# Optimization experiments

Hardware: AMD Instinct MI355X
Metric: run time of the kernel (lower is better)

The kernel has to match this reference:

```python
import jax, jax.numpy as jnp
from jax import lax
import numpy as np
import math

B, H, W = 4, 64, 64
D_MODEL, D_STATE, D_CONV, EXPAND, K = 96, 16, 3, 2, 4
D_INNER = EXPAND * D_MODEL          # 192
DT_RANK = math.ceil(D_MODEL / 16)   # 6


def setup_inputs() -> dict:
    key = jax.random.key(0)
    ks = jax.random.split(key, 12)
    s = 0.02
    rgb = jax.random.normal(ks[0], (B, H, W, D_MODEL), jnp.float32)
    t = jax.random.normal(ks[1], (B, H, W, D_MODEL), jnp.float32)
    in_proj1_w = jax.random.normal(ks[2], (2 * D_INNER, D_MODEL), jnp.float32) * s
    in_proj2_w = jax.random.normal(ks[3], (2 * D_INNER, D_MODEL), jnp.float32) * s
    conv1_w = jax.random.normal(ks[4], (D_INNER, 1, D_CONV, D_CONV), jnp.float32) * s
    conv1_b = jnp.zeros((D_INNER,), jnp.float32)
    conv2_w = jax.random.normal(ks[5], (D_INNER, 1, D_CONV, D_CONV), jnp.float32) * s
    conv2_b = jnp.zeros((D_INNER,), jnp.float32)
    x_proj_weight = jax.random.normal(ks[6], (K, DT_RANK + 2 * D_STATE, D_INNER), jnp.float32) * s
    lim = DT_RANK ** -0.5
    dt_projs_weight = jax.random.uniform(ks[7], (K, D_INNER, DT_RANK), jnp.float32, -lim, lim)
    dt = jnp.exp(jax.random.uniform(ks[8], (K, D_INNER), jnp.float32)
                 * (math.log(0.1) - math.log(0.001)) + math.log(0.001))
    dt = jnp.clip(dt, 1e-4, None)
    dt_projs_bias = dt + jnp.log(-jnp.expm1(-dt))  # inverse softplus
    A_logs = jnp.tile(jnp.log(jnp.arange(1, D_STATE + 1, dtype=jnp.float32))[None], (K * D_INNER, 1))
    Ds = jnp.ones((K * D_INNER,), jnp.float32)
    norm1_w = jnp.ones((D_INNER,), jnp.float32); norm1_b = jnp.zeros((D_INNER,), jnp.float32)
    norm2_w = jnp.ones((D_INNER,), jnp.float32); norm2_b = jnp.zeros((D_INNER,), jnp.float32)
    out_proj1_w = jax.random.normal(ks[9], (D_MODEL, D_INNER), jnp.float32) * s
    out_proj2_w = jax.random.normal(ks[10], (D_MODEL, D_INNER), jnp.float32) * s
    return dict(rgb=rgb, t=t, in_proj1_w=in_proj1_w, in_proj2_w=in_proj2_w,
                conv1_w=conv1_w, conv1_b=conv1_b, conv2_w=conv2_w, conv2_b=conv2_b,
                x_proj_weight=x_proj_weight, dt_projs_weight=dt_projs_weight,
                dt_projs_bias=dt_projs_bias, A_logs=A_logs, Ds=Ds,
                norm1_w=norm1_w, norm1_b=norm1_b, norm2_w=norm2_w, norm2_b=norm2_b,
                out_proj1_w=out_proj1_w, out_proj2_w=out_proj2_w)


def _dwconv(x, w, b):
    # x: (B, C, H, W), depthwise 3x3, padding=1
    y = lax.conv_general_dilated(x, w, (1, 1), 'SAME',
                                 feature_group_count=x.shape[1],
                                 dimension_numbers=('NCHW', 'OIHW', 'NCHW'))
    return y + b[None, :, None, None]


def _ln(x, w, b, eps=1e-5):
    m = x.mean(-1, keepdims=True)
    v = ((x - m) ** 2).mean(-1, keepdims=True)
    return (x - m) / jnp.sqrt(v + eps) * w + b


def _cross_scan(x):
    # x: (B, C, H, W) -> (B, 4, C, L): row-major, col-major, and their reverses
    Bz, C, Hh, Ww = x.shape
    L = Hh * Ww
    xr = x.reshape(Bz, C, L)
    xt = x.transpose(0, 1, 3, 2).reshape(Bz, C, L)
    xh = jnp.stack([xr, xt], 1)                        # (B,2,C,L)
    return jnp.concatenate([xh, jnp.flip(xh, -1)], 1)  # (B,4,C,L)


def _cross_merge(y, Hh, Ww):
    # y: (B, 4, C, L) -> (B, C, L); undo scan directions then sum
    Bz, _, C, L = y.shape
    inv = jnp.flip(y[:, 2:4], -1)                      # (B,2,C,L)
    wh = y[:, 1].reshape(Bz, C, Ww, Hh).transpose(0, 1, 3, 2).reshape(Bz, C, L)
    invwh = inv[:, 1].reshape(Bz, C, Ww, Hh).transpose(0, 1, 3, 2).reshape(Bz, C, L)
    return y[:, 0] + inv[:, 0] + wh + invwh


def _selective_scan(u, delta, A, Bs, Cs, Ds, delta_bias):
    # u, delta: (B, K, C, L2); A: (K, C, N); Bs, Cs: (B, K, N, L2); Ds: (K, C)
    Bz, Kk, C, L2 = u.shape
    N = A.shape[-1]
    delta = jax.nn.softplus(delta + delta_bias[None, :, :, None])

    def step(h, inp):
        d_l, u_l, B_l, C_l = inp               # (B,K,C),(B,K,C),(B,K,N),(B,K,N)
        dA = jnp.exp(d_l[..., None] * A[None])            # (B,K,C,N)
        dBu = (d_l * u_l)[..., None] * B_l[:, :, None, :]  # (B,K,C,N)
        h = h * dA + dBu
        y = jnp.einsum('bkcn,bkn->bkc', h, C_l)
        return h, y

    h0 = jnp.zeros((Bz, Kk, C, N), u.dtype)
    seq = (delta.transpose(3, 0, 1, 2), u.transpose(3, 0, 1, 2),
           Bs.transpose(3, 0, 1, 2), Cs.transpose(3, 0, 1, 2))
    _, ys = lax.scan(step, h0, seq)            # (L2, B, K, C)
    y = ys.transpose(1, 2, 3, 0)               # (B, K, C, L2)
    return y + u * Ds[None, :, :, None]


def _forward_core(x1, x2, x_proj_weight, dt_projs_weight, dt_projs_bias, A_logs, Ds):
    # x1, x2: (B, C, H, W)
    Bz, C, Hh, Ww = x1.shape
    L = Hh * Ww
    rgb4 = _cross_scan(x1)                     # (B,4,C,L)
    t4 = _cross_scan(x2)
    # interleave modalities along sequence: [..., rgb_i, t_i, ...] length 2L
    xs = jnp.stack([rgb4, t4], -1).reshape(Bz, K, C, 2 * L)
    x_dbl = jnp.einsum('bkdl,kcd->bkcl', xs, x_proj_weight)
    dts, Bm, Cm = jnp.split(x_dbl, [DT_RANK, DT_RANK + D_STATE], axis=2)
    dts = jnp.einsum('bkrl,kdr->bkdl', dts, dt_projs_weight)   # (B,K,C,2L)
    As = -jnp.exp(A_logs.astype(jnp.float32)).reshape(K, C, D_STATE)
    y = _selective_scan(xs, dts, As, Bm, Cm, Ds.reshape(K, C), dt_projs_bias)
    y = y.reshape(Bz, K, C, L, 2)
    y_rgb = _cross_merge(y[..., 0], Hh, Ww)    # (B,C,L)
    y_t = _cross_merge(y[..., 1], Hh, Ww)
    return y_rgb, y_t


def reference(rgb, t, in_proj1_w, in_proj2_w, conv1_w, conv1_b, conv2_w, conv2_b,
              x_proj_weight, dt_projs_weight, dt_projs_bias, A_logs, Ds,
              norm1_w, norm1_b, norm2_w, norm2_b, out_proj1_w, out_proj2_w):
    Bz, Hh, Ww, _ = rgb.shape
    x1, z1 = jnp.split(rgb @ in_proj1_w.T, 2, -1)
    x2, z2 = jnp.split(t @ in_proj2_w.T, 2, -1)
    x1 = jax.nn.silu(_dwconv(x1.transpose(0, 3, 1, 2), conv1_w, conv1_b))
    x2 = jax.nn.silu(_dwconv(x2.transpose(0, 3, 1, 2), conv2_w, conv2_b))
    y_rgb, y_t = _forward_core(x1, x2, x_proj_weight, dt_projs_weight,
                               dt_projs_bias, A_logs, Ds)
    y_rgb = _ln(y_rgb.transpose(0, 2, 1).reshape(Bz, Hh, Ww, D_INNER), norm1_w, norm1_b)
    y_t = _ln(y_t.transpose(0, 2, 1).reshape(Bz, Hh, Ww, D_INNER), norm2_w, norm2_b)
    out1 = (y_rgb * jax.nn.silu(z1)) @ out_proj1_w.T
    out2 = (y_t * jax.nn.silu(z2)) @ out_proj2_w.T
    return out1, out2
```

## Files before the change

### kernel.cpp

```cpp
#include <hip/hip_runtime.h>
#include <math.h>

#define BB   4
#define LL   4096
#define L2T  8192
#define DM   96
#define CI   192
#define KD   4
#define NN   16
#define RR   6
#define BKT  16
#define SS   128
#define TT   64
#define DBLS 40

#define OFF_XPRE1 0
#define OFF_XPRE2 3145728
#define OFF_Z1    6291456
#define OFF_Z2    9437184
#define OFF_X1C   12582912
#define OFF_X2C   15728640
#define OFF_DBL   18874368
#define OFF_MERG  24117248
#define OFF_DSUM  30408704

__global__ __launch_bounds__(256)
void k_inproj(const float* __restrict__ rgb, const float* __restrict__ tin,
              const float* __restrict__ w1, const float* __restrict__ w2,
              float* __restrict__ xp1, float* __restrict__ xp2,
              float* __restrict__ zz1, float* __restrict__ zz2) {
  int mb = blockIdx.x;
  int nb = blockIdx.y;
  int m  = blockIdx.z;
  const float* in = m ? tin : rgb;
  const float* w  = (m ? w2 : w1) + nb * 96 * DM;
  __shared__ float As[64][100];
  __shared__ float Ws[96][98];
  int t = threadIdx.x;
  const float4* asrc = (const float4*)(in + (size_t)mb * 64 * DM);
  for (int i = t; i < 1536; i += 256) {
    int r = i / 24, kk = (i % 24) * 4;
    *(float4*)&As[r][kk] = asrc[i];
  }
  const float2* wsrc = (const float2*)w;
  for (int i = t; i < 4608; i += 256) {
    int r = i / 48, kk = (i % 48) * 2;
    *(float2*)&Ws[r][kk] = wsrc[i];
  }
  __syncthreads();
  int tc = t & 15, tr = t >> 4;
  float acc[4][6] = {};
  for (int k = 0; k < 96; k += 2) {
    float2 a[4], b[6];
#pragma unroll
    for (int i = 0; i < 4; i++) a[i] = *(const float2*)&As[tr * 4 + i][k];
#pragma unroll
    for (int j = 0; j < 6; j++) b[j] = *(const float2*)&Ws[tc * 6 + j][k];
#pragma unroll
    for (int i = 0; i < 4; i++)
#pragma unroll
      for (int j = 0; j < 6; j++) {
        acc[i][j] = fmaf(a[i].x, b[j].x, acc[i][j]);
        acc[i][j] = fmaf(a[i].y, b[j].y, acc[i][j]);
      }
  }
  float* dst = (nb < 2) ? (m ? xp2 : xp1) : (m ? zz2 : zz1);
  int colbase = (nb & 1) * 96 + tc * 6;
#pragma unroll
  for (int i = 0; i < 4; i++) {
    size_t bl = (size_t)mb * 64 + tr * 4 + i;
#pragma unroll
    for (int j = 0; j < 6; j++)
      dst[bl * CI + colbase + j] = acc[i][j];
  }
}

__global__ __launch_bounds__(256)
void k_conv(const float* __restrict__ xp1, const float* __restrict__ xp2,
            const float* __restrict__ c1w, const float* __restrict__ c1b,
            const float* __restrict__ c2w, const float* __restrict__ c2b,
            float* __restrict__ o1, float* __restrict__ o2) {
  int m = blockIdx.y;
  const float* in = m ? xp2 : xp1;
  const float* cw = m ? c2w : c1w;
  const float* cb = m ? c2b : c1b;
  float* out = m ? o2 : o1;
  int idx = blockIdx.x * 256 + threadIdx.x;
  int c = idx % CI;
  int bl = idx / CI;
  int b = bl / LL, l = bl % LL;
  int hh = l >> 6, ww = l & 63;
  float a = cb[c];
#pragma unroll
  for (int di = 0; di < 3; di++) {
    int h2 = hh + di - 1;
    if ((unsigned)h2 >= 64u) continue;
#pragma unroll
    for (int dj = 0; dj < 3; dj++) {
      int w2 = ww + dj - 1;
      if ((unsigned)w2 >= 64u) continue;
      a = fmaf(in[(b * LL + h2 * 64 + w2) * CI + c], cw[c * 9 + di * 3 + dj], a);
    }
  }
  out[idx] = a / (1.f + __expf(-a));
}

__global__ __launch_bounds__(256)
void k_dbl(const float* __restrict__ x1c, const float* __restrict__ x2c,
           const float* __restrict__ wx, float* __restrict__ dbl) {
  int pt = blockIdx.x;
  int bk = blockIdx.y;
  int b = bk >> 2, k = bk & 3;
  __shared__ float As[64][100];
  __shared__ float Ws[40][100];
  int t = threadIdx.x;
  int tc = t & 7, tr = t >> 3;
  float acc[2][5] = {};
  for (int kc = 0; kc < 2; kc++) {
    if (kc) __syncthreads();
    for (int i = t; i < 1536; i += 256) {
      int r = i / 24, kk = (i % 24) * 4;
      int l2 = pt * 64 + r;
      int mm = l2 & 1, l = l2 >> 1;
      int lt = (k >= 2) ? (LL - 1 - l) : l;
      int sp = (k & 1) ? (((lt & 63) << 6) | (lt >> 6)) : lt;
      const float* src = (mm ? x2c : x1c) + ((size_t)(b * LL + sp)) * CI + kc * 96;
      *(float4*)&As[r][kk] = *(const float4*)(src + kk);
    }
    for (int i = t; i < 960; i += 256) {
      int r = i / 24, kk = (i % 24) * 4;
      float4 v;
      if (r < 38) v = *(const float4*)&wx[(size_t)(k * 38 + r) * CI + kc * 96 + kk];
      else        v = float4{0.f, 0.f, 0.f, 0.f};
      *(float4*)&Ws[r][kk] = v;
    }
    __syncthreads();
    for (int kk2 = 0; kk2 < 96; kk2 += 2) {
      float2 a[2], bv[5];
#pragma unroll
      for (int i = 0; i < 2; i++) a[i] = *(const float2*)&As[tr * 2 + i][kk2];
#pragma unroll
      for (int j = 0; j < 5; j++) bv[j] = *(const float2*)&Ws[tc * 5 + j][kk2];
#pragma unroll
      for (int i = 0; i < 2; i++)
#pragma unroll
        for (int j = 0; j < 5; j++) {
          acc[i][j] = fmaf(a[i].x, bv[j].x, acc[i][j]);
          acc[i][j] = fmaf(a[i].y, bv[j].y, acc[i][j]);
        }
    }
  }
#pragma unroll
  for (int i = 0; i < 2; i++) {
    size_t row = (size_t)bk * L2T + pt * 64 + tr * 2 + i;
#pragma unroll
    for (int j = 0; j < 5; j++) {
      int cc = tc * 5 + j;
      if (cc < 38) dbl[row * DBLS + cc] = acc[i][j];
    }
  }
}

template<int PASS>
__global__ __launch_bounds__(192)
void k_scan(const float* __restrict__ x1c, const float* __restrict__ x2c,
            const float* __restrict__ dbl,
            const float* __restrict__ dtw, const float* __restrict__ dtb,
            const float* __restrict__ alogs, const float* __restrict__ dsv,
            float* __restrict__ hend, float* __restrict__ dsum,
            const float* __restrict__ hin, float* __restrict__ merged) {
  int bid = blockIdx.x;
  int s  = bid & (SS - 1);
  int bk = bid >> 7;
  int b = bk >> 2, kdir = bk & 3;
  int c = threadIdx.x;
  int kc = kdir * CI + c;

  float w2r0 = dtw[kc * RR + 0], w2r1 = dtw[kc * RR + 1], w2r2 = dtw[kc * RR + 2];
  float w2r3 = dtw[kc * RR + 3], w2r4 = dtw[kc * RR + 4], w2r5 = dtw[kc * RR + 5];
  float bias = dtb[kc];
  float Dv   = (PASS == 2) ? dsv[kc] : 0.f;
  float Areg[NN];
#pragma unroll
  for (int n = 0; n < NN; n++) Areg[n] = -__expf(alogs[kc * NN + n]);
  float A1 = Areg[0];
  int ok = 1;
#pragma unroll
  for (int n = 1; n < NN; n++) {
    float want = A1 * (float)(n + 1);
    if (!(fabsf(Areg[n] - want) <= fabsf(want) * 1e-3f + 1e-6f)) ok = 0;
  }
  const bool structured = (__all(ok) != 0);

  float h[NN];
  if (PASS == 2) {
    int base = ((s * BKT + bk) * CI + c) * NN;
#pragma unroll
    for (int n = 0; n < NN; n++) h[n] = hin[base + n];
  } else {
#pragma unroll
    for (int n = 0; n < NN; n++) h[n] = 0.f;
  }
  float dacc = 0.f;

  const float4* dp4 = (const float4*)(dbl + (size_t)(bk * L2T + s * TT) * DBLS);
  const float* u1b = x1c + (size_t)b * LL * CI + c;
  const float* u2b = x2c + (size_t)b * LL * CI + c;

  auto spmap = [&](int l) -> int {
    int lt = (kdir >= 2) ? (LL - 1 - l) : l;
    return (kdir & 1) ? (((lt & 63) << 6) | (lt >> 6)) : lt;
  };

  auto loadrow = [&](float4* Q, int t) {
    const float4* r4 = dp4 + t * 10;
    Q[0] = r4[0]; Q[1] = r4[1]; Q[2] = r4[2];
    Q[3] = r4[3]; Q[4] = r4[4]; Q[5] = r4[5];
    if (PASS == 2) { Q[6] = r4[6]; Q[7] = r4[7]; Q[8] = r4[8]; Q[9] = r4[9]; }
  };

#define DG(Q, i) ((i & 3) == 0 ? Q[(i) >> 2].x : (i & 3) == 1 ? Q[(i) >> 2].y : (i & 3) == 2 ? Q[(i) >> 2].z : Q[(i) >> 2].w)

  auto step = [&](const float4* Q, float u, float& y) {
    float x = bias;
    x = fmaf(DG(Q, 0), w2r0, x); x = fmaf(DG(Q, 1), w2r1, x); x = fmaf(DG(Q, 2), w2r2, x);
    x = fmaf(DG(Q, 3), w2r3, x); x = fmaf(DG(Q, 4), w2r4, x); x = fmaf(DG(Q, 5), w2r5, x);
    float delta = (x > 15.f) ? x : __logf(1.f + __expf(x));
    float du = delta * u;
    float y0 = 0.f, y1 = 0.f, y2 = 0.f, y3 = 0.f;
    if (structured) {
      float r  = __expf(delta * A1);
      float r2 = r * r, r3 = r2 * r, r4 = r2 * r2;
      float r6 = r4 * r2, r8 = r4 * r4;
      float pw[NN];
      pw[0] = r;       pw[1] = r2;      pw[2] = r3;      pw[3] = r4;
      pw[4] = r4 * r;  pw[5] = r6;      pw[6] = r4 * r3; pw[7] = r8;
      pw[8] = r8 * r;  pw[9] = r8 * r2; pw[10] = r8 * r3; pw[11] = r8 * r4;
      pw[12] = r8 * pw[4]; pw[13] = r8 * r6; pw[14] = r8 * pw[6]; pw[15] = r8 * r8;
#pragma unroll
      for (int n = 0; n < NN; n++) {
        h[n] = fmaf(h[n], pw[n], du * DG(Q, 6 + n));
        if (PASS == 2) {
          float* yp = (n & 2) ? ((n & 1) ? &y3 : &y2) : ((n & 1) ? &y1 : &y0);
          *yp = fmaf(h[n], DG(Q, 22 + n), *yp);
        }
      }
    } else {
#pragma unroll
      for (int n = 0; n < NN; n++) {
        float dA = __expf(delta * Areg[n]);
        h[n] = fmaf(h[n], dA, du * DG(Q, 6 + n));
        if (PASS == 2) {
          float* yp = (n & 2) ? ((n & 1) ? &y3 : &y2) : ((n & 1) ? &y1 : &y0);
          *yp = fmaf(h[n], DG(Q, 22 + n), *yp);
        }
      }
    }
    if (PASS == 1) dacc += delta;
    else y = fmaf(u, Dv, (y0 + y1) + (y2 + y3));
  };

  int l0 = (s * TT) >> 1;
  float4 qA[10], qB[10];
  int spC = spmap(l0);
  float u1C = u1b[(size_t)spC * CI];
  float u2C = u2b[(size_t)spC * CI];
  loadrow(qA, 0);
  int spN = 0; float u1N = 0.f, u2N = 0.f;
#pragma unroll 1
  for (int t = 0; t < TT; t += 2) {
    loadrow(qB, t + 1);
    if (t + 2 < TT) {
      spN = spmap(l0 + (t >> 1) + 1);
      u1N = u1b[(size_t)spN * CI];
      u2N = u2b[(size_t)spN * CI];
    }
    float ya, yb;
    step(qA, u1C, ya);
    if (t + 2 < TT) loadrow(qA, t + 2);
    step(qB, u2C, yb);
    if (PASS == 2) {
      float* mrow = merged + (size_t)(b * LL + spC) * (2 * CI) + c;
      atomicAdd(mrow, ya);
      atomicAdd(mrow + CI, yb);
    }
    spC = spN; u1C = u1N; u2C = u2N;
  }
#undef DG

  if (PASS == 1) {
    int base = ((s * BKT + bk) * CI + c) * NN;
#pragma unroll
    for (int n = 0; n < NN; n++) hend[base + n] = h[n];
    if (c < CI) dsum[(s * BKT + bk) * CI + c] = dacc;
  }
}

__global__ __launch_bounds__(256)
void k_prop(const float* __restrict__ hend, const float* __restrict__ dsum,
            const float* __restrict__ alogs, float* __restrict__ hin) {
  int idx = blockIdx.x * 256 + threadIdx.x;
  int n = idx & 15;
  int rest = idx >> 4;
  int c = rest % CI;
  int bk = rest / CI;
  int k = bk & 3;
  float A = -__expf(alogs[(k * CI + c) * NN + n]);
  float h = 0.f;
  for (int s = 0; s < SS; s++) {
    int cell = (s * BKT + bk) * CI + c;
    hin[cell * NN + n] = h;
    float ap = __expf(A * dsum[cell]);
    h = h * ap + hend[cell * NN + n];
  }
}

__global__ __launch_bounds__(192)
void k_lngate(float* __restrict__ merged,
              const float* __restrict__ z1, const float* __restrict__ z2,
              const float* __restrict__ n1w, const float* __restrict__ n1b,
              const float* __restrict__ n2w, const float* __restrict__ n2b) {
  int bid = blockIdx.x;
  int m = bid & 1;
  int bl = bid >> 1;
  int c = threadIdx.x;
  float v = merged[(size_t)bid * CI + c];
  float s1 = v, s2 = v * v;
  for (int o = 32; o > 0; o >>= 1) {
    s1 += __shfl_xor(s1, o);
    s2 += __shfl_xor(s2, o);
  }
  __shared__ float red[2][3];
  int wv = threadIdx.x >> 6, ln = threadIdx.x & 63;
  if (ln == 0) { red[0][wv] = s1; red[1][wv] = s2; }
  __syncthreads();
  float S1 = red[0][0] + red[0][1] + red[0][2];
  float S2 = red[1][0] + red[1][1] + red[1][2];
  float mean = S1 * (1.f / CI);
  float var = S2 * (1.f / CI) - mean * mean;
  float rstd = rsqrtf(var + 1e-5f);
  const float* nw = m ? n2w : n1w;
  const float* nb = m ? n2b : n1b;
  float vn = (v - mean) * rstd * nw[c] + nb[c];
  float z = (m ? z2 : z1)[(size_t)bl * CI + c];
  float g = vn * (z / (1.f + __expf(-z)));
  merged[(size_t)bid * CI + c] = g;
}

__global__ __launch_bounds__(256)
void k_outproj(const float* __restrict__ g,
               const float* __restrict__ w1, const float* __restrict__ w2,
               float* __restrict__ out) {
  int mb = blockIdx.x;
  int m  = blockIdx.y;
  const float* w = m ? w2 : w1;
  __shared__ float As[64][100];
  __shared__ float Ws[96][98];
  int t = threadIdx.x;
  int tc = t & 15, tr = t >> 4;
  float acc[4][6] = {};
  for (int kc = 0; kc < 2; kc++) {
    if (kc) __syncthreads();
    for (int i = t; i < 1536; i += 256) {
      int r = i / 24, kk = (i % 24) * 4;
      *(float4*)&As[r][kk] =
          *(const float4*)&g[((size_t)(mb * 64 + r) * 2 + m) * CI + kc * 96 + kk];
    }
    for (int i = t; i < 4608; i += 256) {
      int r = i / 48, kk = (i % 48) * 2;
      *(float2*)&Ws[r][kk] = *(const float2*)&w[(size_t)r * CI + kc * 96 + kk];
    }
    __syncthreads();
    for (int k = 0; k < 96; k += 2) {
      float2 a[4], b[6];
#pragma unroll
      for (int i = 0; i < 4; i++) a[i] = *(const float2*)&As[tr * 4 + i][k];
#pragma unroll
      for (int j = 0; j < 6; j++) b[j] = *(const float2*)&Ws[tc * 6 + j][k];
#pragma unroll
      for (int i = 0; i < 4; i++)
#pragma unroll
        for (int j = 0; j < 6; j++) {
          acc[i][j] = fmaf(a[i].x, b[j].x, acc[i][j]);
          acc[i][j] = fmaf(a[i].y, b[j].y, acc[i][j]);
        }
    }
  }
  float* outp = out + (size_t)m * (BB * LL * DM);
#pragma unroll
  for (int i = 0; i < 4; i++) {
    size_t bl = (size_t)mb * 64 + tr * 4 + i;
#pragma unroll
    for (int j = 0; j < 6; j++)
      outp[bl * DM + tc * 6 + j] = acc[i][j];
  }
}

extern "C" void kernel_launch(void* const* d_in, const int* in_sizes, int n_in,
                              void* d_out, int out_size, void* d_ws, size_t ws_size,
                              hipStream_t stream) {
  const float* rgb = (const float*)d_in[0];
  const float* tin = (const float*)d_in[1];
  const float* ip1 = (const float*)d_in[2];
  const float* ip2 = (const float*)d_in[3];
  const float* c1w = (const float*)d_in[4];
  const float* c1b = (const float*)d_in[5];
  const float* c2w = (const float*)d_in[6];
  const float* c2b = (const float*)d_in[7];
  const float* wx  = (const float*)d_in[8];
  const float* dtw = (const float*)d_in[9];
  const float* dtb = (const float*)d_in[10];
  const float* alg = (const float*)d_in[11];
  const float* Dsp = (const float*)d_in[12];
  const float* n1w = (const float*)d_in[13];
  const float* n1b = (const float*)d_in[14];
  const float* n2w = (const float*)d_in[15];
  const float* n2b = (const float*)d_in[16];
  const float* op1 = (const float*)d_in[17];
  const float* op2 = (const float*)d_in[18];

  float* ws = (float*)d_ws;
  float* xp1 = ws + OFF_XPRE1;
  float* xp2 = ws + OFF_XPRE2;
  float* z1  = ws + OFF_Z1;
  float* z2  = ws + OFF_Z2;
  float* x1c = ws + OFF_X1C;
  float* x2c = ws + OFF_X2C;
  float* dbl = ws + OFF_DBL;
  float* mg  = ws + OFF_MERG;
  float* dsm = ws + OFF_DSUM;
  float* he  = ws + OFF_MERG;
  float* hi  = ws + OFF_XPRE1;
  float* out = (float*)d_out;

  k_inproj<<<dim3(256, 4, 2), 256, 0, stream>>>(rgb, tin, ip1, ip2, xp1, xp2, z1, z2);
  k_conv<<<dim3(12288, 2), 256, 0, stream>>>(xp1, xp2, c1w, c1b, c2w, c2b, x1c, x2c);
  k_dbl<<<dim3(128, 16), 256, 0, stream>>>(x1c, x2c, wx, dbl);
  k_scan<1><<<SS * BKT, 192, 0, stream>>>(x1c, x2c, dbl, dtw, dtb, alg, Dsp, he, dsm, hi, mg);
  k_prop<<<192, 256, 0, stream>>>(he, dsm, alg, hi);
  hipMemsetAsync(mg, 0, (size_t)6291456 * sizeof(float), stream);
  k_scan<2><<<SS * BKT, 192, 0, stream>>>(x1c, x2c, dbl, dtw, dtb, alg, Dsp, he, dsm, hi, mg);
  k_lngate<<<BB * LL * 2, 192, 0, stream>>>(mg, z1, z2, n1w, n1b, n2w, n2b);
  k_outproj<<<dim3(256, 2), 256, 0, stream>>>(mg, op1, op2, out);
}
```

Baseline: 434.3 us.

## Split scan state dimension across two thread halves per channel

Each scan block now uses 384 threads: two halves handle state indices 0-7 and 8-15 for the same channel. This halves per-thread register state and serial FMA work, which should raise occupancy and parallelism. The cost is that each half recomputes delta, reloads the dbl rows and u values, and issues its own atomicAdd partial-output, so atomic traffic on the merged buffer doubles. The D*u term is added only by the first half, which keeps the result correct.

```diff
diff --git a/kernel.cpp b/kernel.cpp
--- a/kernel.cpp
+++ b/kernel.cpp
@@ -23,6 +23,8 @@
 #define OFF_DBL   18874368
 #define OFF_MERG  24117248
 #define OFF_DSUM  30408704
+
+template<int V> struct ic { static constexpr int value = V; };
 
 __global__ __launch_bounds__(256)
 void k_inproj(const float* __restrict__ rgb, const float* __restrict__ tin,
@@ -162,7 +164,7 @@
 }
 
 template<int PASS>
-__global__ __launch_bounds__(192)
+__global__ __launch_bounds__(384)
 void k_scan(const float* __restrict__ x1c, const float* __restrict__ x2c,
             const float* __restrict__ dbl,
             const float* __restrict__ dtw, const float* __restrict__ dtb,
@@ -173,35 +175,26 @@
   int s  = bid & (SS - 1);
   int bk = bid >> 7;
   int b = bk >> 2, kdir = bk & 3;
-  int c = threadIdx.x;
+  int tid = threadIdx.x;
+  int half = tid / 192;
+  int c = tid % 192;
   int kc = kdir * CI + c;
 
   float w2r0 = dtw[kc * RR + 0], w2r1 = dtw[kc * RR + 1], w2r2 = dtw[kc * RR + 2];
   float w2r3 = dtw[kc * RR + 3], w2r4 = dtw[kc * RR + 4], w2r5 = dtw[kc * RR + 5];
   float bias = dtb[kc];
-  float Dv   = (PASS == 2) ? dsv[kc] : 0.f;
-  float Areg[NN];
-#pragma unroll
-  for (int n = 0; n < NN; n++) Areg[n] = -__expf(alogs[kc * NN + n]);
-  float A1 = Areg[0];
+  float Dv   = (PASS == 2 && half == 0) ? dsv[kc] : 0.f;
+  float a16[NN];
+#pragma unroll
+  for (int n = 0; n < NN; n++) a16[n] = -__expf(alogs[kc * NN + n]);
+  float A1 = a16[0];
   int ok = 1;
 #pragma unroll
   for (int n = 1; n < NN; n++) {
     float want = A1 * (float)(n + 1);
-    if (!(fabsf(Areg[n] - want) <= fabsf(want) * 1e-3f + 1e-6f)) ok = 0;
+    if (!(fabsf(a16[n] - want) <= fabsf(want) * 1e-3f + 1e-6f)) ok = 0;
   }
   const bool structured = (__all(ok) != 0);
-
-  float h[NN];
-  if (PASS == 2) {
-    int base = ((s * BKT + bk) * CI + c) * NN;
-#pragma unroll
-    for (int n = 0; n < NN; n++) h[n] = hin[base + n];
-  } else {
-#pragma unroll
-    for (int n = 0; n < NN; n++) h[n] = 0.f;
-  }
-  float dacc = 0.f;
 
   const float4* dp4 = (const float4*)(dbl + (size_t)(bk * L2T + s * TT) * DBLS);
   const float* u1b = x1c + (size_t)b * LL * CI + c;
@@ -221,79 +214,104 @@
 
 #define DG(Q, i) ((i & 3) == 0 ? Q[(i) >> 2].x : (i & 3) == 1 ? Q[(i) >> 2].y : (i & 3) == 2 ? Q[(i) >> 2].z : Q[(i) >> 2].w)
 
-  auto step = [&](const float4* Q, float u, float& y) {
-    float x = bias;
-    x = fmaf(DG(Q, 0), w2r0, x); x = fmaf(DG(Q, 1), w2r1, x); x = fmaf(DG(Q, 2), w2r2, x);
-    x = fmaf(DG(Q, 3), w2r3, x); x = fmaf(DG(Q, 4), w2r4, x); x = fmaf(DG(Q, 5), w2r5, x);
-    float delta = (x > 15.f) ? x : __logf(1.f + __expf(x));
-    float du = delta * u;
-    float y0 = 0.f, y1 = 0.f, y2 = 0.f, y3 = 0.f;
-    if (structured) {
-      float r  = __expf(delta * A1);
-      float r2 = r * r, r3 = r2 * r, r4 = r2 * r2;
-      float r6 = r4 * r2, r8 = r4 * r4;
-      float pw[NN];
-      pw[0] = r;       pw[1] = r2;      pw[2] = r3;      pw[3] = r4;
-      pw[4] = r4 * r;  pw[5] = r6;      pw[6] = r4 * r3; pw[7] = r8;
-      pw[8] = r8 * r;  pw[9] = r8 * r2; pw[10] = r8 * r3; pw[11] = r8 * r4;
-      pw[12] = r8 * pw[4]; pw[13] = r8 * r6; pw[14] = r8 * pw[6]; pw[15] = r8 * r8;
-#pragma unroll
-      for (int n = 0; n < NN; n++) {
-        h[n] = fmaf(h[n], pw[n], du * DG(Q, 6 + n));
-        if (PASS == 2) {
-          float* yp = (n & 2) ? ((n & 1) ? &y3 : &y2) : ((n & 1) ? &y1 : &y0);
-          *yp = fmaf(h[n], DG(Q, 22 + n), *yp);
+  auto run = [&](auto nb0c) {
+    constexpr int NB0 = decltype(nb0c)::value;
+    float Areg[8];
+#pragma unroll
+    for (int j = 0; j < 8; j++) Areg[j] = a16[NB0 + j];
+    float h[8];
+    if (PASS == 2) {
+      int base = ((s * BKT + bk) * CI + c) * NN + NB0;
+#pragma unroll
+      for (int j = 0; j < 8; j++) h[j] = hin[base + j];
+    } else {
+#pragma unroll
+      for (int j = 0; j < 8; j++) h[j] = 0.f;
+    }
+    float dacc = 0.f;
+
+    auto step = [&](const float4* Q, float u, float& y) {
+      float x = bias;
+      x = fmaf(DG(Q, 0), w2r0, x); x = fmaf(DG(Q, 1), w2r1, x); x = fmaf(DG(Q, 2), w2r2, x);
+      x = fmaf(DG(Q, 3), w2r3, x); x = fmaf(DG(Q, 4), w2r4, x); x = fmaf(DG(Q, 5), w2r5, x);
+      float delta = (x > 15.f) ? x : __logf(1.f + __expf(x));
+      float du = delta * u;
+      float y0 = 0.f, y1 = 0.f;
+      if (structured) {
+        float r  = __expf(delta * A1);
+        float r2 = r * r, r3 = r2 * r, r4 = r2 * r2;
+        float r5 = r4 * r, r6 = r4 * r2, r7 = r4 * r3, r8 = r4 * r4;
+        float pw[8];
+        if constexpr (NB0 == 0) {
+          pw[0] = r;  pw[1] = r2; pw[2] = r3; pw[3] = r4;
+          pw[4] = r5; pw[5] = r6; pw[6] = r7; pw[7] = r8;
+        } else {
+          pw[0] = r8 * r;  pw[1] = r8 * r2; pw[2] = r8 * r3; pw[3] = r8 * r4;
+          pw[4] = r8 * r5; pw[5] = r8 * r6; pw[6] = r8 * r7; pw[7] = r8 * r8;
+        }
+#pragma unroll
+        for (int j = 0; j < 8; j++) {
+          h[j] = fmaf(h[j], pw[j], du * DG(Q, 6 + NB0 + j));
+          if (PASS == 2) {
+            if (j & 1) y1 = fmaf(h[j], DG(Q, 22 + NB0 + j), y1);
+            else       y0 = fmaf(h[j], DG(Q, 22 + NB0 + j), y0);
+          }
+        }
+      } else {
+#pragma unroll
+        for (int j = 0; j < 8; j++) {
+          float dA = __expf(delta * Areg[j]);
+          h[j] = fmaf(h[j], dA, du * DG(Q, 6 + NB0 + j));
+          if (PASS == 2) {
+            if (j & 1) y1 = fmaf(h[j], DG(Q, 22 + NB0 + j), y1);
+            else       y0 = fmaf(h[j], DG(Q, 22 + NB0 + j), y0);
+          }
         }
       }
-    } else {
-#pragma unroll
-      for (int n = 0; n < NN; n++) {
-        float dA = __expf(delta * Areg[n]);
-        h[n] = fmaf(h[n], dA, du * DG(Q, 6 + n));
-        if (PASS == 2) {
-          float* yp = (n & 2) ? ((n & 1) ? &y3 : &y2) : ((n & 1) ? &y1 : &y0);
-          *yp = fmaf(h[n], DG(Q, 22 + n), *yp);
-        }
+      if (PASS == 1) dacc += delta;
+      else y = fmaf(u, Dv, y0 + y1);
+    };
+
+    int l0 = (s * TT) >> 1;
+    float4 qA[10], qB[10];
+    int spC = spmap(l0);
+    float u1C = u1b[(size_t)spC * CI];
+    float u2C = u2b[(size_t)spC * CI];
+    loadrow(qA, 0);
+    int spN = 0; float u1N = 0.f, u2N = 0.f;
+#pragma unroll 1
+    for (int t = 0; t < TT; t += 2) {
+      loadrow(qB, t + 1);
+      if (t + 2 < TT) {
+        spN = spmap(l0 + (t >> 1) + 1);
+        u1N = u1b[(size_t)spN * CI];
+        u2N = u2b[(size_t)spN * CI];
       }
-    }
-    if (PASS == 1) dacc += delta;
-    else y = fmaf(u, Dv, (y0 + y1) + (y2 + y3));
+      float ya, yb;
+      step(qA, u1C, ya);
+      if (t + 2 < TT) loadrow(qA, t + 2);
+      step(qB, u2C, yb);
+      if (PASS == 2) {
+        float* mrow = merged + (size_t)(b * LL + spC) * (2 * CI) + c;
+        atomicAdd(mrow, ya);
+        atomicAdd(mrow + CI, yb);
+      }
+      spC = spN; u1C = u1N; u2C = u2N;
+    }
+
+    if (PASS == 1) {
+      int base = ((s * BKT + bk) * CI + c) * NN + NB0;
+#pragma unroll
+      for (int j = 0; j < 8; j++) hend[base + j] = h[j];
+      if constexpr (NB0 == 0) {
+        dsum[(s * BKT + bk) * CI + c] = dacc;
+      }
+    }
   };
 
-  int l0 = (s * TT) >> 1;
-  float4 qA[10], qB[10];
-  int spC = spmap(l0);
-  float u1C = u1b[(size_t)spC * CI];
-  float u2C = u2b[(size_t)spC * CI];
-  loadrow(qA, 0);
-  int spN = 0; float u1N = 0.f, u2N = 0.f;
-#pragma unroll 1
-  for (int t = 0; t < TT; t += 2) {
-    loadrow(qB, t + 1);
-    if (t + 2 < TT) {
-      spN = spmap(l0 + (t >> 1) + 1);
-      u1N = u1b[(size_t)spN * CI];
-      u2N = u2b[(size_t)spN * CI];
-    }
-    float ya, yb;
-    step(qA, u1C, ya);
-    if (t + 2 < TT) loadrow(qA, t + 2);
-    step(qB, u2C, yb);
-    if (PASS == 2) {
-      float* mrow = merged + (size_t)(b * LL + spC) * (2 * CI) + c;
-      atomicAdd(mrow, ya);
-      atomicAdd(mrow + CI, yb);
-    }
-    spC = spN; u1C = u1N; u2C = u2N;
-  }
+  if (half == 0) run(ic<0>{});
+  else           run(ic<8>{});
 #undef DG
-
-  if (PASS == 1) {
-    int base = ((s * BKT + bk) * CI + c) * NN;
-#pragma unroll
-    for (int n = 0; n < NN; n++) hend[base + n] = h[n];
-    if (c < CI) dsum[(s * BKT + bk) * CI + c] = dacc;
-  }
 }
 
 __global__ __launch_bounds__(256)
@@ -436,10 +454,10 @@
   k_inproj<<<dim3(256, 4, 2), 256, 0, stream>>>(rgb, tin, ip1, ip2, xp1, xp2, z1, z2);
   k_conv<<<dim3(12288, 2), 256, 0, stream>>>(xp1, xp2, c1w, c1b, c2w, c2b, x1c, x2c);
   k_dbl<<<dim3(128, 16), 256, 0, stream>>>(x1c, x2c, wx, dbl);
-  k_scan<1><<<SS * BKT, 192, 0, stream>>>(x1c, x2c, dbl, dtw, dtb, alg, Dsp, he, dsm, hi, mg);
+  k_scan<1><<<SS * BKT, 384, 0, stream>>>(x1c, x2c, dbl, dtw, dtb, alg, Dsp, he, dsm, hi, mg);
   k_prop<<<192, 256, 0, stream>>>(he, dsm, alg, hi);
   hipMemsetAsync(mg, 0, (size_t)6291456 * sizeof(float), stream);
-  k_scan<2><<<SS * BKT, 192, 0, stream>>>(x1c, x2c, dbl, dtw, dtb, alg, Dsp, he, dsm, hi, mg);
+  k_scan<2><<<SS * BKT, 384, 0, stream>>>(x1c, x2c, dbl, dtw, dtb, alg, Dsp, he, dsm, hi, mg);
   k_lngate<<<BB * LL * 2, 192, 0, stream>>>(mg, z1, z2, n1w, n1b, n2w, n2b);
   k_outproj<<<dim3(256, 2), 256, 0, stream>>>(mg, op1, op2, out);
 }
```

Measured after the change: 523.8 us. 20.6% more time.
